# Performance work log

Measured on AMD Instinct MI355X. Metric: run time of the kernel, lower is better.

## Reference

```python
import jax, jax.numpy as jnp
import numpy as np
from jax import lax

B, T, L, H, K, NL, NB = 32, 512, 2048, 512, 3, 2, 256
PAD = (K - 1) // 2
EPS = 1e-5


def _predictor_params(key):
    k1, k2 = jax.random.split(key)
    s = 1.0 / np.sqrt(H * K).astype(np.float32)
    return dict(
        conv_w=jax.random.normal(k1, (NL, H, H, K), jnp.float32) * s,
        conv_b=jnp.zeros((NL, H), jnp.float32),
        ln_g=jnp.ones((NL, H), jnp.float32),
        ln_b=jnp.zeros((NL, H), jnp.float32),
        lin_w=jax.random.normal(k2, (H, 1), jnp.float32) * 0.02,
        lin_b=jnp.zeros((1,), jnp.float32),
    )


def setup_inputs():
    key = jax.random.key(0)
    ks = jax.random.split(key, 8)
    inp = {
        'x': jax.random.normal(ks[0], (B, T, H), jnp.float32),
        'src_mask': jnp.zeros((B, T), bool),
        'duration_target': jax.random.randint(ks[1], (B, T), 0, 8, jnp.int32),
        'pitch_target': jax.random.normal(ks[2], (B, T), jnp.float32),
        'energy_target': jax.random.uniform(ks[3], (B, T), jnp.float32),
        'max_len': L,
    }
    for name, k in zip(('dur', 'pit', 'en'), ks[4:7]):
        for p, v in _predictor_params(k).items():
            inp[name + '_' + p] = v
    inp['pitch_bins'] = jnp.linspace(-3.0, 3.0, NB - 1)
    inp['energy_bins'] = jnp.linspace(0.0, 1.0, NB - 1)
    k1, k2 = jax.random.split(ks[7])
    inp['pitch_emb'] = jax.random.normal(k1, (NB, H), jnp.float32) * 0.02
    inp['energy_emb'] = jax.random.normal(k2, (NB, H), jnp.float32) * 0.02
    return inp


def _layer_norm(h, g, b):
    m = jnp.mean(h, -1, keepdims=True)
    v = jnp.var(h, -1, keepdims=True)
    return (h - m) * lax.rsqrt(v + EPS) * g + b


def _predictor(x, cw, cb, lg, lb, lw, lbias, mask):
    # stack of [Conv1d(k=3,same) -> ReLU -> LayerNorm] x NL, then Linear -> 1
    out = x
    for i in range(NL):
        h = lax.conv_general_dilated(out.transpose(0, 2, 1), cw[i], (1,), [(PAD, PAD)],
                                     dimension_numbers=('NCH', 'OIH', 'NCH'))
        h = h.transpose(0, 2, 1) + cb[i]  # [B, T, H]
        out = _layer_norm(jax.nn.relu(h), lg[i], lb[i])
    out = (out @ lw)[..., 0] + lbias[0]  # [B, T]
    return jnp.where(mask, 0.0, out)


def _length_regulate(x, duration, max_len):
    # vectorized equivalent of the per-token expand+concat+pad loop
    csum = jnp.cumsum(duration, axis=1)                     # [B, T]
    frames = jnp.arange(max_len)                            # [L]
    idx = jax.vmap(lambda c: jnp.searchsorted(c, frames, side='right'))(csum)  # [B, L]
    idx = jnp.clip(idx, 0, x.shape[1] - 1)
    out = jnp.take_along_axis(x, idx[:, :, None], axis=1)   # [B, L, H]
    mel_len = jnp.minimum(csum[:, -1], max_len)             # [B]
    out = out * (frames[None, :] < mel_len[:, None])[..., None]
    return out, mel_len


def reference(x, src_mask, duration_target, pitch_target, energy_target, max_len,
              dur_conv_w, dur_conv_b, dur_ln_g, dur_ln_b, dur_lin_w, dur_lin_b,
              pit_conv_w, pit_conv_b, pit_ln_g, pit_ln_b, pit_lin_w, pit_lin_b,
              en_conv_w, en_conv_b, en_ln_g, en_ln_b, en_lin_w, en_lin_b,
              pitch_bins, energy_bins, pitch_emb, energy_emb):
    log_d = _predictor(x, dur_conv_w, dur_conv_b, dur_ln_g, dur_ln_b, dur_lin_w, dur_lin_b, src_mask)
    pitch_pred = _predictor(x, pit_conv_w, pit_conv_b, pit_ln_g, pit_ln_b, pit_lin_w, pit_lin_b, src_mask)
    energy_pred = _predictor(x, en_conv_w, en_conv_b, en_ln_g, en_ln_b, en_lin_w, en_lin_b, src_mask)
    # torch.bucketize(target, bins) (right=False) == searchsorted side='left'
    p_emb = pitch_emb[jnp.searchsorted(pitch_bins, pitch_target, side='left')]
    e_emb = energy_emb[jnp.searchsorted(energy_bins, energy_target, side='left')]
    x2 = x + p_emb + e_emb
    out, mel_len = _length_regulate(x2, duration_target, max_len)
    return (out, pitch_pred, energy_pred, log_d, mel_len)
```

## Files before the change

kernel.cpp:

```cpp
#include <hip/hip_runtime.h>
#include <hip/hip_bf16.h>

#define B_ 32
#define T_ 512
#define TP_ 514
#define L_ 2048
#define H_ 512
#define NRR (B_*T_)
#define KC_ 1536
#define NB_ 256
#define EPS_ 1e-5f
#define XPE ((size_t)B_ * TP_ * H_)
#define WSEC 196608

typedef __bf16 bf16;
typedef __bf16 bf16x8 __attribute__((ext_vector_type(8)));
typedef float f32x4 __attribute__((ext_vector_type(4)));

static const size_t WC_BYTES  = (size_t)6 * H_ * KC_ * 2;
static const size_t XP_BYTES  = XPE * 2;
static const size_t Y_BYTES   = (size_t)3 * NRR * H_ * 2;

__device__ __forceinline__ void gload16(const void* g, void* l) {
    __builtin_amdgcn_global_load_lds(
        (const __attribute__((address_space(1))) unsigned int*)g,
        (__attribute__((address_space(3))) unsigned int*)l, 16, 0, 0);
}

__global__ void k_prep_wc(const float* __restrict__ wd, const float* __restrict__ wp,
                          const float* __restrict__ we, bf16* __restrict__ wc) {
    int e = blockIdx.x * 256 + threadIdx.x;
    if (e >= 6 * H_ * KC_) return;
    int sec = e / WSEC, r = e % WSEC;
    int m = sec >> 2, colblk = sec & 3;
    int j  = r & 7;
    int l  = (r >> 3) & 63;
    int n  = (r >> 9) & 3;
    int wn = (r >> 11) & 1;
    int kk = (r >> 12) & 1;
    int t13 = r >> 13;
    int tap = t13 % 3, hc = t13 / 3;
    int o = colblk * 128 + wn * 64 + n * 16 + (l & 15);
    int c = hc * 64 + kk * 32 + (l >> 4) * 8 + j;
    int p = m >> 1, i = m & 1;
    const float* w = (p == 0) ? wd : (p == 1 ? wp : we);
    wc[e] = (bf16)w[((size_t)(i * H_ + o) * H_ + c) * 3 + tap];
}

__global__ void k_pad(const float* __restrict__ x, bf16* __restrict__ xp0,
                      bf16* __restrict__ xp1) {
    int wid = threadIdx.x >> 6, lane = threadIdx.x & 63;
    int row = blockIdx.x * 4 + wid;
    int b = row / TP_, tp = row % TP_;
    bf16* d0 = xp0 + (size_t)row * H_ + lane * 8;
    if (tp == 0 || tp == TP_ - 1) {
        bf16x8 z;
#pragma unroll
        for (int i = 0; i < 8; ++i) z[i] = (bf16)0.0f;
        *(bf16x8*)d0 = z;
#pragma unroll
        for (int p = 0; p < 3; ++p)
            *(bf16x8*)(xp1 + p * XPE + (size_t)row * H_ + lane * 8) = z;
    } else {
        const f32x4* p = (const f32x4*)(x + ((size_t)(b * T_ + tp - 1)) * H_ + lane * 8);
        f32x4 u = p[0], v = p[1];
        bf16x8 o;
        o[0] = (bf16)u[0]; o[1] = (bf16)u[1]; o[2] = (bf16)u[2]; o[3] = (bf16)u[3];
        o[4] = (bf16)v[0]; o[5] = (bf16)v[1]; o[6] = (bf16)v[2]; o[7] = (bf16)v[3];
        *(bf16x8*)d0 = o;
    }
}

__global__ void k_scan(const int* __restrict__ dur, int* __restrict__ csum,
                       float* __restrict__ mel_out) {
    int b = blockIdx.x, t = threadIdx.x;
    __shared__ int s[T_];
    s[t] = dur[b * T_ + t];
    __syncthreads();
    for (int off = 1; off < T_; off <<= 1) {
        int v = (t >= off) ? s[t - off] : 0;
        __syncthreads();
        s[t] += v;
        __syncthreads();
    }
    csum[b * T_ + t] = s[t];
    if (t == T_ - 1) mel_out[b] = (float)((s[t] < L_) ? s[t] : L_);
}

__global__ void k_gather(const float* __restrict__ x, const float* __restrict__ pemb,
                         const float* __restrict__ eemb, const float* __restrict__ pt,
                         const float* __restrict__ et, const float* __restrict__ pbins,
                         const float* __restrict__ ebins, const int* __restrict__ csum,
                         float* __restrict__ out) {
    int bi = blockIdx.x;
    int b  = bi >> 9;
    int l0 = (bi & 511) << 2;
    __shared__ int cs[T_];
    __shared__ float pb[NB_ - 1], eb[NB_ - 1];
    cs[threadIdx.x]       = csum[b * T_ + threadIdx.x];
    cs[threadIdx.x + 256] = csum[b * T_ + threadIdx.x + 256];
    if (threadIdx.x < NB_ - 1) {
        pb[threadIdx.x] = pbins[threadIdx.x];
        eb[threadIdx.x] = ebins[threadIdx.x];
    }
    __syncthreads();
    int wid = threadIdx.x >> 6, lane = threadIdx.x & 63;
    int l = l0 + wid;
    int mel = cs[T_ - 1]; if (mel > L_) mel = L_;
    float* op = out + ((size_t)(b * L_ + l)) * H_ + lane * 8;
    if (l >= mel) {
        f32x4 z = {0.f, 0.f, 0.f, 0.f};
        ((f32x4*)op)[0] = z;
        ((f32x4*)op)[1] = z;
        return;
    }
    int lo = 0, hi = T_;
    while (lo < hi) { int mid = (lo + hi) >> 1; if (cs[mid] <= l) lo = mid + 1; else hi = mid; }
    int idx = (lo < T_ - 1) ? lo : (T_ - 1);
    int rr = b * T_ + idx;
    float pv = pt[rr], ev = et[rr];
    int pi, ei;
    { int a = 0, c = NB_ - 1; while (a < c) { int mid = (a + c) >> 1; if (pb[mid] < pv) a = mid + 1; else c = mid; } pi = a; }
    { int a = 0, c = NB_ - 1; while (a < c) { int mid = (a + c) >> 1; if (eb[mid] < ev) a = mid + 1; else c = mid; } ei = a; }
    const f32x4* xp = (const f32x4*)(x    + (size_t)rr * H_ + lane * 8);
    const f32x4* pp = (const f32x4*)(pemb + (size_t)pi * H_ + lane * 8);
    const f32x4* ep = (const f32x4*)(eemb + (size_t)ei * H_ + lane * 8);
    ((f32x4*)op)[0] = xp[0] + pp[0] + ep[0];
    ((f32x4*)op)[1] = xp[1] + pp[1] + ep[1];
}

template<int LAYER>
__global__ __launch_bounds__(256)
void k_gemm(const bf16* __restrict__ Xp, const bf16* __restrict__ Wall,
            const float* __restrict__ cb0, const float* __restrict__ cb1,
            const float* __restrict__ cb2, bf16* __restrict__ Y) {
    __shared__ bf16 lA[136 * 64];

    int bid = blockIdx.x;
    int xcd = bid & 7, idx = bid >> 3;
    int colblk = idx >> 4;
    int rowblk = xcd * 16 + (idx & 15);
    int p  = colblk >> 2;
    int oB = (colblk & 3) * 128;
    int rowBase = rowblk * 128;

    const bf16* A = (LAYER == 0) ? Xp : (Xp + (size_t)p * XPE);
    const bf16* Wsec = Wall + (size_t)((2 * p + LAYER) * 4 + (colblk & 3)) * WSEC;
    const float* cbp  = (p == 0) ? cb0 : (p == 1 ? cb1 : cb2);
    const float* bias = cbp + LAYER * H_;

    int tid = threadIdx.x;
    int wid = tid >> 6, lane = tid & 63;
    int wm = wid >> 1, wn = wid & 1;
    int lr = lane & 15, kq = lane >> 4;
    int rsub = lane >> 3;
    int csw  = ((lane & 7) ^ rsub) << 3;
    int b = rowBase >> 9, t0 = rowBase & (T_ - 1);
    const bf16* Abase = A + ((size_t)(b * TP_ + t0)) * H_;
    const bf16* Wlane = Wsec + (size_t)wn * 2048 + lane * 8;

    f32x4 acc[4][4];
#pragma unroll
    for (int m = 0; m < 4; ++m)
#pragma unroll
        for (int n = 0; n < 4; ++n) acc[m][n] = (f32x4){0.f, 0.f, 0.f, 0.f};

    for (int s = 0; s < 8; ++s) {
        int c0 = s * 64;
#pragma unroll
        for (int q = 0; q < 5; ++q) {
            int g = q * 4 + wid;
            if (g < 17)
                gload16(Abase + (size_t)(g * 8 + rsub) * H_ + c0 + csw, &lA[g * 8 * 64]);
        }
        const bf16* Wh = Wlane + (size_t)s * 24576;
        __syncthreads();

#pragma unroll
        for (int tap = 0; tap < 3; ++tap) {
            bf16x8 af[4][2], bfr[4][2];
            int ka = (lr + tap) & 7;
#pragma unroll
            for (int n = 0; n < 4; ++n)
#pragma unroll
                for (int kk = 0; kk < 2; ++kk)
                    bfr[n][kk] = *(const bf16x8*)&Wh[((size_t)(tap * 2 + kk) * 2) * 2048 +
                                                     n * 512];
#pragma unroll
            for (int m = 0; m < 4; ++m)
#pragma unroll
                for (int kk = 0; kk < 2; ++kk)
                    af[m][kk] = *(const bf16x8*)&lA[(wm * 64 + m * 16 + lr + tap) * 64 +
                                                    ((((kk * 4 + kq) ^ ka)) << 3)];
#pragma unroll
            for (int m = 0; m < 4; ++m)
#pragma unroll
                for (int n = 0; n < 4; ++n)
#pragma unroll
                    for (int kk = 0; kk < 2; ++kk)
                        acc[m][n] = __builtin_amdgcn_mfma_f32_16x16x32_bf16(
                            af[m][kk], bfr[n][kk], acc[m][n], 0, 0, 0);
        }
        __syncthreads();
    }

#pragma unroll
    for (int n = 0; n < 4; ++n) {
        int o = oB + wn * 64 + n * 16 + lr;
        float bi = bias[o];
#pragma unroll
        for (int m = 0; m < 4; ++m) {
            int row = rowBase + wm * 64 + m * 16 + 4 * kq;
#pragma unroll
            for (int r = 0; r < 4; ++r)
                Y[((size_t)p * NRR + row + r) * H_ + o] = (bf16)fmaxf(acc[m][n][r] + bi, 0.f);
        }
    }
}

__global__ void k_ln_store(const bf16* __restrict__ Yin,
                           const float* __restrict__ g0, const float* __restrict__ g1,
                           const float* __restrict__ g2,
                           const float* __restrict__ bb0, const float* __restrict__ bb1,
                           const float* __restrict__ bb2, bf16* __restrict__ xp1) {
    int wid = threadIdx.x >> 6, lane = threadIdx.x & 63;
    int rg = blockIdx.x * 4 + wid;
    int p = rg >> 14, r = rg & (NRR - 1);
    const float* g   = (p == 0) ? g0 : (p == 1 ? g1 : g2);
    const float* bta = (p == 0) ? bb0 : (p == 1 ? bb1 : bb2);
    bf16x8 a = *(const bf16x8*)(Yin + ((size_t)p * NRR + r) * H_ + lane * 8);
    float f[8];
#pragma unroll
    for (int i = 0; i < 8; ++i) f[i] = (float)a[i];
    float s1 = 0.f, s2 = 0.f;
#pragma unroll
    for (int i = 0; i < 8; ++i) { s1 += f[i]; s2 += f[i] * f[i]; }
    for (int m = 1; m < 64; m <<= 1) { s1 += __shfl_xor(s1, m); s2 += __shfl_xor(s2, m); }
    float mean = s1 * (1.f / H_);
    float var  = s2 * (1.f / H_) - mean * mean;
    float rs   = rsqrtf(var + EPS_);
    const f32x4* gp = (const f32x4*)g;
    const f32x4* bp = (const f32x4*)bta;
    f32x4 ga = gp[lane * 2], gb = gp[lane * 2 + 1];
    f32x4 ba = bp[lane * 2], bbv = bp[lane * 2 + 1];
    bf16x8 o;
    o[0] = (bf16)((f[0] - mean) * rs * ga[0] + ba[0]);
    o[1] = (bf16)((f[1] - mean) * rs * ga[1] + ba[1]);
    o[2] = (bf16)((f[2] - mean) * rs * ga[2] + ba[2]);
    o[3] = (bf16)((f[3] - mean) * rs * ga[3] + ba[3]);
    o[4] = (bf16)((f[4] - mean) * rs * gb[0] + bbv[0]);
    o[5] = (bf16)((f[5] - mean) * rs * gb[1] + bbv[1]);
    o[6] = (bf16)((f[6] - mean) * rs * gb[2] + bbv[2]);
    o[7] = (bf16)((f[7] - mean) * rs * gb[3] + bbv[3]);
    int bb = r >> 9, t = r & (T_ - 1);
    *(bf16x8*)(xp1 + (size_t)p * XPE + ((size_t)(bb * TP_ + t + 1)) * H_ + lane * 8) = o;
}

__global__ void k_ln_linear(const bf16* __restrict__ Yin,
                            const float* __restrict__ g0, const float* __restrict__ g1,
                            const float* __restrict__ g2,
                            const float* __restrict__ bb0, const float* __restrict__ bb1,
                            const float* __restrict__ bb2,
                            const float* __restrict__ w0p, const float* __restrict__ w1p,
                            const float* __restrict__ w2p,
                            const float* __restrict__ lb0, const float* __restrict__ lb1,
                            const float* __restrict__ lb2,
                            const unsigned char* __restrict__ mask,
                            float* __restrict__ o0, float* __restrict__ o1,
                            float* __restrict__ o2) {
    int wid = threadIdx.x >> 6, lane = threadIdx.x & 63;
    int rg = blockIdx.x * 4 + wid;
    int p = rg >> 14, r = rg & (NRR - 1);
    const float* g   = ((p == 0) ? g0 : (p == 1 ? g1 : g2)) + H_;
    const float* bta = ((p == 0) ? bb0 : (p == 1 ? bb1 : bb2)) + H_;
    const float* lw  = (p == 0) ? w0p : (p == 1 ? w1p : w2p);
    const float* lb  = (p == 0) ? lb0 : (p == 1 ? lb1 : lb2);
    float*       op  = (p == 0) ? o0 : (p == 1 ? o1 : o2);
    bf16x8 a = *(const bf16x8*)(Yin + ((size_t)p * NRR + r) * H_ + lane * 8);
    float f[8];
#pragma unroll
    for (int i = 0; i < 8; ++i) f[i] = (float)a[i];
    float s1 = 0.f, s2 = 0.f;
#pragma unroll
    for (int i = 0; i < 8; ++i) { s1 += f[i]; s2 += f[i] * f[i]; }
    for (int m = 1; m < 64; m <<= 1) { s1 += __shfl_xor(s1, m); s2 += __shfl_xor(s2, m); }
    float mean = s1 * (1.f / H_);
    float var  = s2 * (1.f / H_) - mean * mean;
    float rs   = rsqrtf(var + EPS_);
    const f32x4* gp = (const f32x4*)g;
    const f32x4* bp = (const f32x4*)bta;
    const f32x4* wp = (const f32x4*)lw;
    f32x4 ga = gp[lane * 2], gb = gp[lane * 2 + 1];
    f32x4 ba = bp[lane * 2], bbv = bp[lane * 2 + 1];
    f32x4 wa = wp[lane * 2], wb = wp[lane * 2 + 1];
    float s = ((f[0] - mean) * rs * ga[0] + ba[0]) * wa[0]
            + ((f[1] - mean) * rs * ga[1] + ba[1]) * wa[1]
            + ((f[2] - mean) * rs * ga[2] + ba[2]) * wa[2]
            + ((f[3] - mean) * rs * ga[3] + ba[3]) * wa[3]
            + ((f[4] - mean) * rs * gb[0] + bbv[0]) * wb[0]
            + ((f[5] - mean) * rs * gb[1] + bbv[1]) * wb[1]
            + ((f[6] - mean) * rs * gb[2] + bbv[2]) * wb[2]
            + ((f[7] - mean) * rs * gb[3] + bbv[3]) * wb[3];
    for (int m = 1; m < 64; m <<= 1) s += __shfl_xor(s, m);
    if (lane == 0) op[r] = mask[r] ? 0.f : (s + lb[0]);
}

extern "C" void kernel_launch(void* const* d_in, const int* in_sizes, int n_in,
                              void* d_out, int out_size, void* d_ws, size_t ws_size,
                              hipStream_t stream) {
    const float* x  = (const float*)d_in[0];
    const unsigned char* mask = (const unsigned char*)d_in[1];
    const int*   dur = (const int*)d_in[2];
    const float* pt  = (const float*)d_in[3];
    const float* et  = (const float*)d_in[4];
    const float* cw[3]    = {(const float*)d_in[6],  (const float*)d_in[12], (const float*)d_in[18]};
    const float* cb[3]    = {(const float*)d_in[7],  (const float*)d_in[13], (const float*)d_in[19]};
    const float* lg[3]    = {(const float*)d_in[8],  (const float*)d_in[14], (const float*)d_in[20]};
    const float* lbn[3]   = {(const float*)d_in[9],  (const float*)d_in[15], (const float*)d_in[21]};
    const float* lw[3]    = {(const float*)d_in[10], (const float*)d_in[16], (const float*)d_in[22]};
    const float* lbias[3] = {(const float*)d_in[11], (const float*)d_in[17], (const float*)d_in[23]};
    const float* pbins = (const float*)d_in[24];
    const float* ebins = (const float*)d_in[25];
    const float* pemb  = (const float*)d_in[26];
    const float* eemb  = (const float*)d_in[27];

    float* out0 = (float*)d_out;
    const size_t OUT0 = (size_t)B_ * L_ * H_;
    float* pitch_out  = out0 + OUT0;
    float* energy_out = pitch_out + NRR;
    float* logd_out   = energy_out + NRR;
    float* mel_out    = logd_out + NRR;

    char* ws = (char*)d_ws;
    bf16*  wc   = (bf16*)ws;
    bf16*  xp0  = (bf16*)(ws + WC_BYTES);
    bf16*  xp1  = (bf16*)(ws + WC_BYTES + XP_BYTES);
    bf16*  y    = (bf16*)(ws + WC_BYTES + 4 * XP_BYTES);
    int*   csum = (int*)(ws + WC_BYTES + 4 * XP_BYTES + Y_BYTES);

    k_prep_wc<<<(6 * H_ * KC_ + 255) / 256, 256, 0, stream>>>(cw[0], cw[1], cw[2], wc);
    k_pad<<<B_ * TP_ / 4, 256, 0, stream>>>(x, xp0, xp1);
    k_scan<<<B_, T_, 0, stream>>>(dur, csum, mel_out);
    k_gather<<<B_ * L_ / 4, 256, 0, stream>>>(x, pemb, eemb, pt, et, pbins, ebins, csum, out0);

    k_gemm<0><<<1536, 256, 0, stream>>>(xp0, wc, cb[0], cb[1], cb[2], y);
    k_ln_store<<<3 * NRR / 4, 256, 0, stream>>>(y, lg[0], lg[1], lg[2],
                                                lbn[0], lbn[1], lbn[2], xp1);
    k_gemm<1><<<1536, 256, 0, stream>>>(xp1, wc, cb[0], cb[1], cb[2], y);
    k_ln_linear<<<3 * NRR / 4, 256, 0, stream>>>(y, lg[0], lg[1], lg[2],
                                                 lbn[0], lbn[1], lbn[2],
                                                 lw[0], lw[1], lw[2],
                                                 lbias[0], lbias[1], lbias[2],
                                                 mask, logd_out, pitch_out, energy_out);
}
```

Measured before the change: 265.2 us.

## Double-buffer LDS A tiles and prefetch weight fragments in conv GEMM

The conv-as-GEMM kernel gets a two-slot LDS buffer for the A tile, so the next K-slice is staged with global_load_lds while the current one feeds MFMAs. Weight fragments are also register double-buffered, with the next tap's B fragments loaded before the current tap's MFMAs. This hides global-load latency behind compute and removes one barrier per step. The cost is twice the LDS footprint and more VGPRs for the B buffers, which can lower occupancy.

```diff
diff --git a/kernel.cpp b/kernel.cpp
--- a/kernel.cpp
+++ b/kernel.cpp
@@ -134,7 +134,7 @@
 void k_gemm(const bf16* __restrict__ Xp, const bf16* __restrict__ Wall,
             const float* __restrict__ cb0, const float* __restrict__ cb1,
             const float* __restrict__ cb2, bf16* __restrict__ Y) {
-    __shared__ bf16 lA[136 * 64];
+    __shared__ bf16 lA[2][136 * 64];
 
     int bid = blockIdx.x;
     int xcd = bid & 7, idx = bid >> 3;
@@ -165,33 +165,43 @@
 #pragma unroll
         for (int n = 0; n < 4; ++n) acc[m][n] = (f32x4){0.f, 0.f, 0.f, 0.f};
 
+    bf16x8 bfr[2][8];
+
+#define STAGE_A(S, D) do { \
+    const bf16* sa_ = Abase + (S) * 64 + csw; \
+    _Pragma("unroll") for (int q_ = 0; q_ < 5; ++q_) { \
+        int g_ = q_ * 4 + wid; \
+        if (g_ < 17) gload16(sa_ + (size_t)(g_ * 8 + rsub) * H_, &lA[D][g_ * 8 * 64]); \
+    } \
+} while (0)
+
+#define LOADB(G, DB) do { \
+    const bf16* pb_ = Wlane + (size_t)((G) / 3) * 24576 + (size_t)((G) % 3) * 8192; \
+    _Pragma("unroll") for (int n_ = 0; n_ < 4; ++n_) { \
+        bfr[DB][n_]     = *(const bf16x8*)&pb_[n_ * 512]; \
+        bfr[DB][4 + n_] = *(const bf16x8*)&pb_[4096 + n_ * 512]; \
+    } \
+} while (0)
+
+    LOADB(0, 0);
+    STAGE_A(0, 0);
+    __syncthreads();
+
+#pragma unroll
     for (int s = 0; s < 8; ++s) {
-        int c0 = s * 64;
-#pragma unroll
-        for (int q = 0; q < 5; ++q) {
-            int g = q * 4 + wid;
-            if (g < 17)
-                gload16(Abase + (size_t)(g * 8 + rsub) * H_ + c0 + csw, &lA[g * 8 * 64]);
-        }
-        const bf16* Wh = Wlane + (size_t)s * 24576;
-        __syncthreads();
-
+        if (s < 7) STAGE_A(s + 1, (s + 1) & 1);
 #pragma unroll
         for (int tap = 0; tap < 3; ++tap) {
-            bf16x8 af[4][2], bfr[4][2];
-            int ka = (lr + tap) & 7;
-#pragma unroll
-            for (int n = 0; n < 4; ++n)
+            const int g = 3 * s + tap;
+            if (g < 23) LOADB(g + 1, (g + 1) & 1);
+            bf16x8 af[4][2];
+            const int ka = (lr + tap) & 7;
+#pragma unroll
+            for (int m = 0; m < 4; ++m)
 #pragma unroll
                 for (int kk = 0; kk < 2; ++kk)
-                    bfr[n][kk] = *(const bf16x8*)&Wh[((size_t)(tap * 2 + kk) * 2) * 2048 +
-                                                     n * 512];
-#pragma unroll
-            for (int m = 0; m < 4; ++m)
-#pragma unroll
-                for (int kk = 0; kk < 2; ++kk)
-                    af[m][kk] = *(const bf16x8*)&lA[(wm * 64 + m * 16 + lr + tap) * 64 +
-                                                    ((((kk * 4 + kq) ^ ka)) << 3)];
+                    af[m][kk] = *(const bf16x8*)&lA[s & 1][(wm * 64 + m * 16 + lr + tap) * 64 +
+                                                           (((kk * 4 + kq) ^ ka) << 3)];
 #pragma unroll
             for (int m = 0; m < 4; ++m)
 #pragma unroll
@@ -199,10 +209,12 @@
 #pragma unroll
                     for (int kk = 0; kk < 2; ++kk)
                         acc[m][n] = __builtin_amdgcn_mfma_f32_16x16x32_bf16(
-                            af[m][kk], bfr[n][kk], acc[m][n], 0, 0, 0);
+                            af[m][kk], bfr[g & 1][kk * 4 + n], acc[m][n], 0, 0, 0);
         }
         __syncthreads();
     }
+#undef STAGE_A
+#undef LOADB
 
 #pragma unroll
     for (int n = 0; n < 4; ++n) {
```

After: 308.7 us. +16.4%, slower.
